# Kernel optimization log

Hardware: AMD Instinct MI355X
Metric: run time of the kernel (lower is better)

Reference implementation:

```python
import jax, jax.numpy as jnp
import numpy as np

EMBED = 1024
HEADS = 16
HEAD_DIM = EMBED // HEADS
SCALE = HEAD_DIM ** -0.5


def setup_inputs() -> dict:
    key = jax.random.key(0)
    ks = jax.random.split(key, 9)
    init = lambda k, shape: jax.random.normal(k, shape, dtype=jnp.float32) * 0.02
    return {
        "hidden_states": jax.random.normal(ks[0], (32, 257, EMBED), dtype=jnp.float32),
        "Wq": init(ks[1], (EMBED, EMBED)), "bq": init(ks[2], (EMBED,)),
        "Wk": init(ks[3], (EMBED, EMBED)), "bk": init(ks[4], (EMBED,)),
        "Wv": init(ks[5], (EMBED, EMBED)), "bv": init(ks[6], (EMBED,)),
        "Wo": init(ks[7], (EMBED, EMBED)), "bo": init(ks[8], (EMBED,)),
    }


def reference(hidden_states, Wq, bq, Wk, bk, Wv, bv, Wo, bo):
    b, t, d = hidden_states.shape
    # projections (torch Linear: x @ W.T + b); scale applied to Q
    q = (hidden_states @ Wq.T + bq) * SCALE
    k = hidden_states @ Wk.T + bk
    v = hidden_states @ Wv.T + bv
    # [b, h, t, hd]
    q = q.reshape(b, t, HEADS, HEAD_DIM).transpose(0, 2, 1, 3)
    k = k.reshape(b, t, HEADS, HEAD_DIM).transpose(0, 2, 1, 3)
    v = v.reshape(b, t, HEADS, HEAD_DIM).transpose(0, 2, 1, 3)
    # attention scores + softmax (dropout p is a no-op in eval mode)
    scores = jnp.einsum("bhqd,bhkd->bhqk", q, k)
    probs = jax.nn.softmax(scores, axis=-1)
    ctx = jnp.einsum("bhqk,bhkd->bhqd", probs, v)
    ctx = ctx.transpose(0, 2, 1, 3).reshape(b, t, d)
    return ctx @ Wo.T + bo
```

## Files before the change

kernel.cpp:

```cpp
#include <hip/hip_runtime.h>


#define B_   32
#define T_   257
#define TP   272
#define H_   16
#define HD_  64
#define D_   1024
#define NTOK 8224
#define BH_  512
#define FRAG_PER_BH 17408

typedef __bf16 bf16;
typedef __bf16 bf16x4 __attribute__((ext_vector_type(4)));
typedef __bf16 bf16x8 __attribute__((ext_vector_type(8)));
typedef short  s16x4  __attribute__((ext_vector_type(4)));
typedef short  s16x8  __attribute__((ext_vector_type(8)));
typedef float  floatx4 __attribute__((ext_vector_type(4)));

static constexpr size_t SZ_XB   = (size_t)NTOK * D_ * 2;
static constexpr size_t SZ_WQKV = (size_t)3 * D_ * D_ * 2;
static constexpr size_t SZ_W    = (size_t)D_ * D_ * 2;
static constexpr size_t SZ_QK   = (size_t)BH_ * FRAG_PER_BH * 2;

static constexpr size_t OFF_XB   = 0;
static constexpr size_t OFF_WQKV = OFF_XB + SZ_XB;
static constexpr size_t OFF_WO   = OFF_WQKV + SZ_WQKV;
static constexpr size_t OFF_Q    = OFF_WO + SZ_W;
static constexpr size_t OFF_K    = OFF_Q + SZ_QK;
static constexpr size_t OFF_V    = OFF_K + SZ_QK;
static constexpr size_t OFF_CTX  = OFF_V + SZ_QK;

#define GLD16(gp, lp)                                                        \
  __builtin_amdgcn_global_load_lds(                                          \
      (const __attribute__((address_space(1))) void*)(gp),                   \
      (__attribute__((address_space(3))) void*)(lp), 16, 0, 0)

__global__ void cast_all_kernel(const float* __restrict__ hs,
                                const float* __restrict__ Wq, const float* __restrict__ Wk,
                                const float* __restrict__ Wv, const float* __restrict__ Wo,
                                bf16* __restrict__ xb, bf16* __restrict__ wqkv,
                                bf16* __restrict__ wob) {
  const int y = blockIdx.y;
  const float* s;
  bf16* d;
  int n4;
  if (y == 0) {
    s = hs; d = xb; n4 = NTOK * D_ / 4;
  } else {
    int z = y - 1;
    s = (z == 0) ? Wq : (z == 1) ? Wk : (z == 2) ? Wv : Wo;
    d = (z < 3) ? wqkv + (size_t)z * D_ * D_ : wob;
    n4 = D_ * D_ / 4;
  }
  int i = blockIdx.x * blockDim.x + threadIdx.x;
  int stride = gridDim.x * blockDim.x;
  for (int idx = i; idx < n4; idx += stride) {
    float4 v = reinterpret_cast<const float4*>(s)[idx];
    bf16x4 o;
    o[0] = (bf16)v.x; o[1] = (bf16)v.y; o[2] = (bf16)v.z; o[3] = (bf16)v.w;
    reinterpret_cast<bf16x4*>(d)[idx] = o;
  }
}



#define KTILE(TT, CC)                                                        \
  do {                                                                       \
    const int ktn_ = ((TT) + 2 < 32) ? (TT) + 2 : 31;                        \
    _Pragma("unroll") for (int mi_ = 0; mi_ < 4; mi_++)                      \
      af[mi_] = *reinterpret_cast<const bf16x8*>(                            \
          smem + (CC) * 8192 + (arow + mi_ * 16) * 32 + qsw);                \
    _Pragma("unroll") for (int nj_ = 0; nj_ < 4; nj_++)                      \
      bfr[nj_] = *reinterpret_cast<const bf16x8*>(                           \
          smem + 16384 + (CC) * 4096 + (brow + nj_ * 16) * 32 + qsw);        \
    asm volatile("s_waitcnt lgkmcnt(0)" ::: "memory");                       \
    __builtin_amdgcn_sched_barrier(0);                                       \
    __builtin_amdgcn_s_barrier();                                            \
    GLD16(aSrc0 + ktn_ * 32, dstA0 + (CC) * 8192);                           \
    GLD16(aSrc1 + ktn_ * 32, dstA1 + (CC) * 8192);                           \
    GLD16(bSrc + ktn_ * 32, dstB + (CC) * 4096);                             \
    __builtin_amdgcn_sched_barrier(0);                                       \
    __builtin_amdgcn_s_setprio(1);                                           \
    _Pragma("unroll") for (int mi_ = 0; mi_ < 4; mi_++)                      \
      _Pragma("unroll") for (int nj_ = 0; nj_ < 4; nj_++)                    \
        acc[mi_][nj_] = __builtin_amdgcn_mfma_f32_16x16x32_bf16(             \
            af[mi_], bfr[nj_], acc[mi_][nj_], 0, 0, 0);                      \
    __builtin_amdgcn_s_setprio(0);                                           \
    asm volatile("s_waitcnt vmcnt(3)" ::: "memory");                         \
    __builtin_amdgcn_s_barrier();                                            \
  } while (0)

__global__ __launch_bounds__(512, 4) void qkv_gemm(
    const bf16* __restrict__ xb, const bf16* __restrict__ wqkv,
    const float* __restrict__ bq, const float* __restrict__ bk,
    const float* __restrict__ bv,
    bf16* __restrict__ Qf, bf16* __restrict__ Kf, bf16* __restrict__ Vf) {
  __shared__ bf16 smem[24576];

  const int linear = blockIdx.x;
  const int mt = linear / 24, nt = linear % 24;
  const int m0 = mt * 256, n0 = nt * 128;
  const int tid = threadIdx.x;
  const int lane = tid & 63, w = tid >> 6;
  const int n15 = lane & 15, quad = lane >> 4;
  const int wr4 = w >> 1, wn = w & 1;

  const int arow = wr4 * 64 + n15;
  const int brow = wn * 64 + n15;
  const int qsw = (quad ^ ((n15 >> 1) & 3)) * 8;

  const int srow = lane >> 2;
  const int sseg = ((lane & 3) ^ ((lane >> 3) & 3)) * 8;
  int gmA0 = m0 + (w * 2 + 0) * 16 + srow; if (gmA0 > NTOK - 1) gmA0 = NTOK - 1;
  int gmA1 = m0 + (w * 2 + 1) * 16 + srow; if (gmA1 > NTOK - 1) gmA1 = NTOK - 1;
  const bf16* aSrc0 = xb + (size_t)gmA0 * D_ + sseg;
  const bf16* aSrc1 = xb + (size_t)gmA1 * D_ + sseg;
  const bf16* bSrc  = wqkv + (size_t)(n0 + w * 16 + srow) * D_ + sseg;
  bf16* dstA0 = smem + (w * 2 + 0) * 512;
  bf16* dstA1 = smem + (w * 2 + 1) * 512;
  bf16* dstB  = smem + 16384 + w * 512;

  floatx4 acc[4][4] = {};
  bf16x8 af[4], bfr[4];

  GLD16(aSrc0, dstA0); GLD16(aSrc1, dstA1); GLD16(bSrc, dstB);
  GLD16(aSrc0 + 32, dstA0 + 8192); GLD16(aSrc1 + 32, dstA1 + 8192);
  GLD16(bSrc + 32, dstB + 4096);
  asm volatile("s_waitcnt vmcnt(3)" ::: "memory");
  __builtin_amdgcn_s_barrier();

  for (int t = 0; t < 32; t += 2) {
    KTILE(t, 0);
    KTILE(t + 1, 1);
  }

  asm volatile("s_waitcnt vmcnt(0)" ::: "memory");
  __builtin_amdgcn_s_barrier();

  const int z = nt >> 3;
  bf16* zdst = (z == 0) ? Qf : (z == 1) ? Kf : Vf;
  const float scale = (z == 0) ? 0.125f : 1.0f;
  const float* bias = (z == 0) ? bq : (z == 1) ? bk : bv;
  const int znb = (nt & 7) * 128;

  for (int h = 0; h < 2; h++) {
    if ((wr4 >> 1) == h) {
      float bvv[4];
#pragma unroll
      for (int nj = 0; nj < 4; nj++)
        bvv[nj] = bias[znb + wn * 64 + nj * 16 + n15];
#pragma unroll
      for (int mi = 0; mi < 4; mi++)
#pragma unroll
        for (int nj = 0; nj < 4; nj++) {
          int colL = wn * 64 + nj * 16 + n15;
#pragma unroll
          for (int r = 0; r < 4; r++) {
            int rowL = (wr4 & 1) * 64 + mi * 16 + quad * 4 + r;
            smem[rowL * 136 + colL] = (bf16)((acc[mi][nj][r] + bvv[nj]) * scale);
          }
        }
    }
    __syncthreads();

    const int mh0 = m0 + h * 128;
    int nU = 0, nA = 0, tgA0 = 0, tA = 0, tEndA = 0, tEndB = 0, bA = 0;
    int span = NTOK - mh0;
    if (span > 0) {
      if (span > 128) span = 128;
      bA = mh0 / T_;
      tA = mh0 - bA * T_;
      tEndA = (tA + span < T_) ? tA + span : T_;
      tgA0 = tA >> 4;
      nA = ((tEndA - 1) >> 4) - tgA0 + 1;
      nU = nA;
      if (tA + span > T_ && bA + 1 < B_) {
        tEndB = tA + span - T_;
        nU += ((tEndB - 1) >> 4) + 1;
      }
    }

    for (int u = w; u < nU * 2; u += 8) {
      int g = u >> 1, hh = u & 1;
      int bb, tg, tlo, thi;
      if (g < nA) {
        bb = bA; tg = tgA0 + g;
        tlo = (tA > tg * 16) ? tA : tg * 16;
        int te = tg * 16 + 16; thi = (te < tEndA) ? te : tEndA;
      } else {
        bb = bA + 1; tg = g - nA; tlo = tg * 16;
        int te = tg * 16 + 16; thi = (te < tEndB) ? te : tEndB;
      }
      const int hgl = (nt & 7) * 2 + hh;
      bf16* gb = zdst + (size_t)(bb * H_ + hgl) * FRAG_PER_BH + tg * 1024;
      const int hc = hh * 64;
      if (z != 2) {
        int ki = lane & 15, dc = lane >> 4;
        int tt = tg * 16 + ki;
        if (tt >= tlo && tt < thi) {
          int rowL = bb * T_ + tt - mh0;
          bf16x8 v0 = *reinterpret_cast<const bf16x8*>(smem + rowL * 136 + hc + dc * 8);
          bf16x8 v1 = *reinterpret_cast<const bf16x8*>(smem + rowL * 136 + hc + 32 + dc * 8);
          *reinterpret_cast<bf16x8*>(gb + dc * 128 + ki * 8) = v0;
          *reinterpret_cast<bf16x8*>(gb + 512 + dc * 128 + ki * 8) = v1;
        }
      } else {
        int q2 = (lane >> 4) & 3, d16 = lane & 15;
        int tb = tg * 16 + q2 * 4;
        bool full = (tb >= tlo) && (tb + 3 < thi);
#pragma unroll
        for (int p = 0; p < 2; p++) {
          bf16x8 vv;
#pragma unroll
          for (int dp = 0; dp < 2; dp++)
#pragma unroll
            for (int ki = 0; ki < 4; ki++) {
              int tt = tb + ki;
              int rr = (bb * T_ + tt - mh0) & 127;
              vv[dp * 4 + ki] = smem[rr * 136 + hc + p * 32 + dp * 16 + d16];
            }
          bf16* cp = gb + (p * 4 + q2) * 128 + d16 * 8;
          if (full) {
            *reinterpret_cast<bf16x8*>(cp) = vv;
          } else {
#pragma unroll
            for (int dp = 0; dp < 2; dp++)
#pragma unroll
              for (int ki = 0; ki < 4; ki++) {
                int tt = tb + ki;
                if (tt >= tlo && tt < thi) cp[dp * 4 + ki] = vv[dp * 4 + ki];
                else if (tt >= T_)         cp[dp * 4 + ki] = (bf16)0.0f;
              }
          }
        }
      }
    }
    __syncthreads();
  }
}

__global__ __launch_bounds__(512) void attn_kernel(
    const bf16* __restrict__ Qf, const bf16* __restrict__ Kf,
    const bf16* __restrict__ Vf, bf16* __restrict__ ctx) {
  __shared__ bf16 smem[34816];

  const int bh = blockIdx.x;
  const int tid = threadIdx.x;
  const int lane = tid & 63, w = tid >> 6;
  const int n15 = lane & 15, quad = lane >> 4;
  const int b = bh >> 4, h = bh & 15;

  const bf16* Qb = Qf + (size_t)bh * FRAG_PER_BH;
  const bf16* Kb = Kf + (size_t)bh * FRAG_PER_BH;
  const bf16* Vb = Vf + (size_t)bh * FRAG_PER_BH;

#pragma unroll
  for (int j = 0; j < 9; j++) {
    int c = j * 8 + w;
    if (c < 68) {
      const bf16* src = (c < 34) ? (Kb + c * 512) : (Vb + (c - 34) * 512);
      GLD16(src + lane * 8, smem + c * 512);
    }
  }
  __syncthreads();
  const bf16* Ksh = smem;
  const bf16* Vsh = smem + 17408;

  const int fo = quad * 128 + n15 * 8;

  for (int qt = w; qt < 17; qt += 8) {
    bf16x8 qb0 = *reinterpret_cast<const bf16x8*>(Qb + qt * 1024 + fo);
    bf16x8 qb1 = *reinterpret_cast<const bf16x8*>(Qb + qt * 1024 + 512 + fo);

    floatx4 s[17];
#pragma unroll
    for (int kt = 0; kt < 17; kt++) {
      bf16x8 ka0 = *reinterpret_cast<const bf16x8*>(Ksh + kt * 1024 + fo);
      bf16x8 ka1 = *reinterpret_cast<const bf16x8*>(Ksh + kt * 1024 + 512 + fo);
      floatx4 c = {};
      c = __builtin_amdgcn_mfma_f32_16x16x32_bf16(ka0, qb0, c, 0, 0, 0);
      c = __builtin_amdgcn_mfma_f32_16x16x32_bf16(ka1, qb1, c, 0, 0, 0);
      s[kt] = c;
    }
    s[16][1] = -1e30f; s[16][2] = -1e30f; s[16][3] = -1e30f;
    if (quad != 0) s[16][0] = -1e30f;

    float m0 = -1e30f;
#pragma unroll
    for (int kt = 0; kt < 17; kt++)
#pragma unroll
      for (int r = 0; r < 4; r++) m0 = fmaxf(m0, s[kt][r]);
    m0 = fmaxf(m0, __shfl_xor(m0, 16));
    m0 = fmaxf(m0, __shfl_xor(m0, 32));

    float sum = 0.f;
    s16x4 pb[17];
#pragma unroll
    for (int kt = 0; kt < 17; kt++) {
      bf16x4 ph;
#pragma unroll
      for (int r = 0; r < 4; r++) {
        float p = __expf(s[kt][r] - m0);
        sum += p;
        ph[r] = (bf16)p;
      }
      pb[kt] = __builtin_bit_cast(s16x4, ph);
    }
    sum += __shfl_xor(sum, 16);
    sum += __shfl_xor(sum, 32);

    floatx4 o[4] = {};
#pragma unroll
    for (int kt = 0; kt < 17; kt++) {
#pragma unroll
      for (int p = 0; p < 2; p++) {
        bf16x8 vv = *reinterpret_cast<const bf16x8*>(
            Vsh + ((kt * 2 + p) * 4 + quad) * 128 + n15 * 8);
        s16x8 v16 = __builtin_bit_cast(s16x8, vv);
        s16x4 vlo = __builtin_shufflevector(v16, v16, 0, 1, 2, 3);
        s16x4 vhi = __builtin_shufflevector(v16, v16, 4, 5, 6, 7);
        o[p * 2]     = __builtin_amdgcn_mfma_f32_16x16x16bf16_1k(vlo, pb[kt], o[p * 2], 0, 0, 0);
        o[p * 2 + 1] = __builtin_amdgcn_mfma_f32_16x16x16bf16_1k(vhi, pb[kt], o[p * 2 + 1], 0, 0, 0);
      }
    }

    int q = qt * 16 + n15;
    if (q < T_) {
      float inv = 1.0f / sum;
      size_t ob = ((size_t)(b * T_ + q)) * D_ + h * 64 + quad * 4;
#pragma unroll
      for (int dt = 0; dt < 4; dt++) {
        bf16x4 ov;
#pragma unroll
        for (int r = 0; r < 4; r++) ov[r] = (bf16)(o[dt][r] * inv);
        *reinterpret_cast<bf16x4*>(ctx + ob + dt * 16) = ov;
      }
    }
  }
}

#define KTILE_O(TT, CC)                                                      \
  do {                                                                       \
    const int ktn_ = ((TT) + 2 < 32) ? (TT) + 2 : 31;                        \
    _Pragma("unroll") for (int i_ = 0; i_ < 4; i_++) {                       \
      af[i_]  = *reinterpret_cast<const bf16x8*>(                            \
          smem + (CC) * 4096 + (wr * 64 + i_ * 16 + n15) * 32 + qsw);        \
      bfr[i_] = *reinterpret_cast<const bf16x8*>(                            \
          smem + 8192 + (CC) * 4096 + (wc * 64 + i_ * 16 + n15) * 32 + qsw); \
    }                                                                        \
    asm volatile("s_waitcnt lgkmcnt(0)" ::: "memory");                       \
    __builtin_amdgcn_sched_barrier(0);                                       \
    __builtin_amdgcn_s_barrier();                                            \
    GLD16(aS0 + ktn_ * 32, dA0 + (CC) * 4096);                               \
    GLD16(aS1 + ktn_ * 32, dA1 + (CC) * 4096);                               \
    GLD16(bS0 + ktn_ * 32, dB0 + (CC) * 4096);                               \
    GLD16(bS1 + ktn_ * 32, dB1 + (CC) * 4096);                               \
    __builtin_amdgcn_sched_barrier(0);                                       \
    __builtin_amdgcn_s_setprio(1);                                           \
    _Pragma("unroll") for (int i_ = 0; i_ < 4; i_++)                         \
      _Pragma("unroll") for (int j_ = 0; j_ < 4; j_++)                       \
        acc[i_][j_] = __builtin_amdgcn_mfma_f32_16x16x32_bf16(               \
            af[i_], bfr[j_], acc[i_][j_], 0, 0, 0);                          \
    __builtin_amdgcn_s_setprio(0);                                           \
    asm volatile("s_waitcnt vmcnt(4)" ::: "memory");                         \
    __builtin_amdgcn_s_barrier();                                            \
  } while (0)

__global__ __launch_bounds__(256) void o_gemm(
    const bf16* __restrict__ ctx, const bf16* __restrict__ wo,
    const float* __restrict__ bo, float* __restrict__ out) {
  __shared__ bf16 smem[16384];

  const int linear = blockIdx.x;
  const int nbase = (linear & 7) * 128;
  const int mbase = (linear >> 3) * 128;
  const int tid = threadIdx.x;
  const int lane = tid & 63;
  const int w = tid >> 6;
  const int wr = w >> 1, wc = w & 1;
  const int n15 = lane & 15, quad = lane >> 4;

  const int lrow = lane >> 2;
  const int lseg = ((lane & 3) ^ ((lane >> 3) & 3)) * 8;
  const int qsw = (quad ^ ((n15 >> 1) & 3)) * 8;

  int gm0 = mbase + w * 32 + lrow;      if (gm0 > NTOK - 1) gm0 = NTOK - 1;
  int gm1 = mbase + w * 32 + 16 + lrow; if (gm1 > NTOK - 1) gm1 = NTOK - 1;
  const bf16* aS0 = ctx + (size_t)gm0 * D_ + lseg;
  const bf16* aS1 = ctx + (size_t)gm1 * D_ + lseg;
  const bf16* bS0 = wo + (size_t)(nbase + w * 32 + lrow) * D_ + lseg;
  const bf16* bS1 = wo + (size_t)(nbase + w * 32 + 16 + lrow) * D_ + lseg;
  bf16* dA0 = smem + (w * 32) * 32;
  bf16* dA1 = smem + (w * 32 + 16) * 32;
  bf16* dB0 = smem + 8192 + (w * 32) * 32;
  bf16* dB1 = smem + 8192 + (w * 32 + 16) * 32;

  floatx4 acc[4][4] = {};
  bf16x8 af[4], bfr[4];

  GLD16(aS0, dA0); GLD16(aS1, dA1); GLD16(bS0, dB0); GLD16(bS1, dB1);
  GLD16(aS0 + 32, dA0 + 4096); GLD16(aS1 + 32, dA1 + 4096);
  GLD16(bS0 + 32, dB0 + 4096); GLD16(bS1 + 32, dB1 + 4096);
  asm volatile("s_waitcnt vmcnt(4)" ::: "memory");
  __builtin_amdgcn_s_barrier();

  for (int t = 0; t < 32; t += 2) {
    KTILE_O(t, 0);
    KTILE_O(t + 1, 1);
  }
  asm volatile("s_waitcnt vmcnt(0)" ::: "memory");

#pragma unroll
  for (int i = 0; i < 4; i++) {
    int rowb = mbase + wr * 64 + i * 16 + quad * 4;
#pragma unroll
    for (int j = 0; j < 4; j++) {
      int col = nbase + wc * 64 + j * 16 + n15;
      float bval = bo[col];
#pragma unroll
      for (int r = 0; r < 4; r++) {
        int m = rowb + r;
        if (m < NTOK) out[(size_t)m * D_ + col] = acc[i][j][r] + bval;
      }
    }
  }
}

extern "C" void kernel_launch(void* const* d_in, const int* in_sizes, int n_in,
                              void* d_out, int out_size, void* d_ws, size_t ws_size,
                              hipStream_t stream) {
  const float* hs = (const float*)d_in[0];
  const float* Wq = (const float*)d_in[1];
  const float* bq = (const float*)d_in[2];
  const float* Wk = (const float*)d_in[3];
  const float* bk = (const float*)d_in[4];
  const float* Wv = (const float*)d_in[5];
  const float* bv = (const float*)d_in[6];
  const float* Wo = (const float*)d_in[7];
  const float* bo = (const float*)d_in[8];

  char* ws = (char*)d_ws;
  bf16* xb   = (bf16*)(ws + OFF_XB);
  bf16* wqkv = (bf16*)(ws + OFF_WQKV);
  bf16* wob  = (bf16*)(ws + OFF_WO);
  bf16* Qfw  = (bf16*)(ws + OFF_Q);
  bf16* Kfw  = (bf16*)(ws + OFF_K);
  bf16* Vfw  = (bf16*)(ws + OFF_V);
  bf16* ctx  = (bf16*)(ws + OFF_CTX);

  cast_all_kernel<<<dim3(512, 5), 256, 0, stream>>>(hs, Wq, Wk, Wv, Wo,
                                                    xb, wqkv, wob);

  qkv_gemm<<<792, 512, 0, stream>>>(xb, wqkv, bq, bk, bv, Qfw, Kfw, Vfw);
  attn_kernel<<<BH_, 512, 0, stream>>>(Qfw, Kfw, Vfw, ctx);
  o_gemm<<<520, 256, 0, stream>>>(ctx, wob, bo, (float*)d_out);
}
```

Before: 278.5 us.

## Replace two-pass softmax with online softmax in attention kernel

Fuses score computation, softmax and PV accumulation into a single loop over key tiles, using a running max with rescaling of the sum and output accumulators. This drops the 17-entry score and probability register arrays, cutting register pressure and possibly raising occupancy. In exchange it adds per-tile cross-lane shuffles, extra exp calls and accumulator rescaling, and it serialises the MFMA chain so less instruction-level parallelism is available.

```diff
diff --git a/kernel.cpp b/kernel.cpp
--- a/kernel.cpp
+++ b/kernel.cpp
@@ -273,7 +273,9 @@
     bf16x8 qb0 = *reinterpret_cast<const bf16x8*>(Qb + qt * 1024 + fo);
     bf16x8 qb1 = *reinterpret_cast<const bf16x8*>(Qb + qt * 1024 + 512 + fo);
 
-    floatx4 s[17];
+    float m_run = -1e30f, sum = 0.f;
+    floatx4 o[4] = {};
+
 #pragma unroll
     for (int kt = 0; kt < 17; kt++) {
       bf16x8 ka0 = *reinterpret_cast<const bf16x8*>(Ksh + kt * 1024 + fo);
@@ -281,38 +283,29 @@
       floatx4 c = {};
       c = __builtin_amdgcn_mfma_f32_16x16x32_bf16(ka0, qb0, c, 0, 0, 0);
       c = __builtin_amdgcn_mfma_f32_16x16x32_bf16(ka1, qb1, c, 0, 0, 0);
-      s[kt] = c;
-    }
-    s[16][1] = -1e30f; s[16][2] = -1e30f; s[16][3] = -1e30f;
-    if (quad != 0) s[16][0] = -1e30f;
-
-    float m0 = -1e30f;
-#pragma unroll
-    for (int kt = 0; kt < 17; kt++)
-#pragma unroll
-      for (int r = 0; r < 4; r++) m0 = fmaxf(m0, s[kt][r]);
-    m0 = fmaxf(m0, __shfl_xor(m0, 16));
-    m0 = fmaxf(m0, __shfl_xor(m0, 32));
-
-    float sum = 0.f;
-    s16x4 pb[17];
-#pragma unroll
-    for (int kt = 0; kt < 17; kt++) {
+      if (kt == 16) {
+        c[1] = -1e30f; c[2] = -1e30f; c[3] = -1e30f;
+        if (quad != 0) c[0] = -1e30f;
+      }
+      float mt = fmaxf(fmaxf(c[0], c[1]), fmaxf(c[2], c[3]));
+      mt = fmaxf(mt, __shfl_xor(mt, 16));
+      mt = fmaxf(mt, __shfl_xor(mt, 32));
+      float m_new = fmaxf(m_run, mt);
+      float rs = __expf(m_run - m_new);
+      sum *= rs;
+#pragma unroll
+      for (int dt = 0; dt < 4; dt++) o[dt] *= rs;
+      m_run = m_new;
+
       bf16x4 ph;
 #pragma unroll
       for (int r = 0; r < 4; r++) {
-        float p = __expf(s[kt][r] - m0);
+        float p = __expf(c[r] - m_new);
         sum += p;
         ph[r] = (bf16)p;
       }
-      pb[kt] = __builtin_bit_cast(s16x4, ph);
-    }
-    sum += __shfl_xor(sum, 16);
-    sum += __shfl_xor(sum, 32);
-
-    floatx4 o[4] = {};
-#pragma unroll
-    for (int kt = 0; kt < 17; kt++) {
+      s16x4 pbk = __builtin_bit_cast(s16x4, ph);
+
 #pragma unroll
       for (int p = 0; p < 2; p++) {
         bf16x8 vv = *reinterpret_cast<const bf16x8*>(
@@ -320,10 +313,13 @@
         s16x8 v16 = __builtin_bit_cast(s16x8, vv);
         s16x4 vlo = __builtin_shufflevector(v16, v16, 0, 1, 2, 3);
         s16x4 vhi = __builtin_shufflevector(v16, v16, 4, 5, 6, 7);
-        o[p * 2]     = __builtin_amdgcn_mfma_f32_16x16x16bf16_1k(vlo, pb[kt], o[p * 2], 0, 0, 0);
-        o[p * 2 + 1] = __builtin_amdgcn_mfma_f32_16x16x16bf16_1k(vhi, pb[kt], o[p * 2 + 1], 0, 0, 0);
-      }
-    }
+        o[p * 2]     = __builtin_amdgcn_mfma_f32_16x16x16bf16_1k(vlo, pbk, o[p * 2], 0, 0, 0);
+        o[p * 2 + 1] = __builtin_amdgcn_mfma_f32_16x16x16bf16_1k(vhi, pbk, o[p * 2 + 1], 0, 0, 0);
+      }
+    }
+
+    sum += __shfl_xor(sum, 16);
+    sum += __shfl_xor(sum, 32);
 
     int q = qt * 16 + n15;
     if (q < T_) {
```

Result: slower. 296.6 us (+6.5%).
